# Performance work log

Hardware: AMD Instinct MI355X
Metric: run time of the kernel (lower is better)

## Reference

```python
import jax, jax.numpy as jnp
import numpy as np

E, H = 1024, 16


def setup_inputs() -> dict:
    key = jax.random.key(0)
    k1, k2, k3, k4 = jax.random.split(key, 4)
    B, L = 4, 2048
    embeddings = jax.random.normal(k1, (B, L, E), dtype=jnp.float32)
    mask = jax.random.randint(k2, (B, L, L), 0, 2) == 1  # True = masked out
    # Params (torch Linear y = x @ W.T; we store already-transposed [in, out])
    W_qkv = jax.random.normal(k3, (E, 3 * E), dtype=jnp.float32) * 0.02
    W_out = jax.random.normal(k4, (E, E), dtype=jnp.float32) * 0.02
    return {"embeddings": embeddings, "mask": mask, "W_qkv": W_qkv, "W_out": W_out}


def reference(embeddings, mask, W_qkv, W_out):
    B, L, E_ = embeddings.shape
    A = E_ // H
    scale = A ** (-0.5)
    qkv = embeddings @ W_qkv                       # [B, L, 3E]
    qkv = qkv.reshape(B, L, H, 3 * A).transpose(0, 2, 1, 3)  # [B, H, L, 3A]
    q, k, v = jnp.split(qkv, 3, axis=-1)           # each [B, H, L, A]
    scores = jnp.einsum('bhqa,bhka->bhqk', q, k) * scale  # [B, H, L, L]
    m = mask[:, None, :, :]                        # [B, 1, L, L]
    fully = jnp.all(m, axis=-1, keepdims=True)     # rows with every key masked
    scores = jnp.where(m, -jnp.inf, scores)
    scores = jnp.where(fully, 0.0, scores)         # keep softmax finite
    attn = jax.nn.softmax(scores, axis=-1)
    attn = jnp.where(fully, 0.0, attn)             # == torch nan_to_num(0)
    values = jnp.einsum('bhqk,bhka->bhqa', attn, v)  # [B, H, L, A]
    values = values.transpose(0, 2, 1, 3).reshape(B, L, E_)
    return values @ W_out
```

## Files before the change

### kernel.cpp

```cpp
#include <hip/hip_runtime.h>
#include <hip/hip_bf16.h>

#define B_   4
#define L_   2048
#define E_   1024
#define H_   16
#define T_   8192
#define K_   1024

typedef __attribute__((ext_vector_type(8))) short bf16x8;
typedef __attribute__((ext_vector_type(4))) float f32x4;

#define CSC_ (0.125f * 1.44269504f)

__device__ __forceinline__ ushort f2b(float f) {
    union { float f; unsigned u; } x; x.f = f;
    unsigned r = (x.u + 0x7fffu + ((x.u >> 16) & 1u)) >> 16;
    return (ushort)r;
}

__device__ __forceinline__ float fexp2(float x) {
#if __has_builtin(__builtin_amdgcn_exp2f)
    return __builtin_amdgcn_exp2f(x);
#else
    return __expf(x * 0.69314718056f);
#endif
}

__device__ __forceinline__ unsigned pack2bf(float a, float b) {
#if __has_builtin(__builtin_amdgcn_cvt_pk_bf16_f32)
    auto t = __builtin_amdgcn_cvt_pk_bf16_f32(a, b);
    return __builtin_bit_cast(unsigned, t);
#else
    unsigned ua = __builtin_bit_cast(unsigned, a) + 0x8000u;
    unsigned ub = __builtin_bit_cast(unsigned, b) + 0x8000u;
    return __builtin_amdgcn_perm(ub, ua, 0x07060302);
#endif
}

#define GLD_LDS16(gp, lp) __builtin_amdgcn_global_load_lds( \
    (const __attribute__((address_space(1))) void*)(gp), \
    (__attribute__((address_space(3))) void*)(lp), 16, 0, 0)

__global__ void detect_mask_layout(const unsigned char* __restrict__ m, int* flag) {
    __shared__ int s;
    if (threadIdx.x == 0) s = 0;
    __syncthreads();
    int found = 0;
    for (int i = threadIdx.x; i < 4096; i += 256)
        if ((i & 3) != 0 && m[i] != 0) found = 1;
    if (found) atomicOr(&s, 1);
    __syncthreads();
    if (threadIdx.x == 0) *flag = s;
}

__global__ void pack_mask(const void* __restrict__ mraw, const int* __restrict__ flag,
                          unsigned long long* __restrict__ bits) {
    int row  = blockIdx.x;
    int lane = threadIdx.x & 63;
    int wave = threadIdx.x >> 6;
    int isByte = *flag;
    const unsigned char* mb = (const unsigned char*)mraw;
    const int*           mi = (const int*)mraw;
    long long base = (long long)row * L_;
    for (int w = wave; w < 32; w += 4) {
        int idx = w * 64 + lane;
        int v = isByte ? (int)mb[base + idx] : mi[base + idx];
        unsigned long long word = __ballot(v == 0);
        if (lane == 0) bits[row * 32 + w] = word;
    }
}

__global__ __launch_bounds__(256) void conv_bf16(const float* __restrict__ in,
                                                 ushort* __restrict__ out) {
    int i = blockIdx.x * 256 + threadIdx.x;
    float4 v = ((const float4*)in)[i];
    uint2 o;
    o.x = (unsigned)f2b(v.x) | ((unsigned)f2b(v.y) << 16);
    o.y = (unsigned)f2b(v.z) | ((unsigned)f2b(v.w) << 16);
    ((uint2*)out)[i] = o;
}

__global__ __launch_bounds__(256) void transpose_conv(const float* __restrict__ in,
        ushort* __restrict__ out, int R, int Cn) {
    __shared__ float t[32][33];
    int c0 = blockIdx.x * 32, r0 = blockIdx.y * 32;
    int x = threadIdx.x & 31, y = threadIdx.x >> 5;
#pragma unroll
    for (int k = 0; k < 4; ++k)
        t[y + k * 8][x] = in[(size_t)(r0 + y + k * 8) * Cn + c0 + x];
    __syncthreads();
#pragma unroll
    for (int k = 0; k < 4; ++k)
        out[(size_t)(c0 + y + k * 8) * R + r0 + x] = f2b(t[x][y + k * 8]);
}

template<int NDIM, int MODE>
__global__ __launch_bounds__(256) void gemm_bf16(
        const ushort* __restrict__ Ab, const ushort* __restrict__ Bt,
        float* __restrict__ Cg, ushort* __restrict__ Qb,
        ushort* __restrict__ Kb, ushort* __restrict__ Vt) {
    __shared__ ushort As[128 * 64];
    __shared__ ushort Bs[128 * 64];
    const int tid = threadIdx.x;
    const int wv = tid >> 6, ln = tid & 63;
    const int bn = blockIdx.x * 128, bm = blockIdx.y * 128;
    const int wm = (wv & 1) * 64, wn = (wv >> 1) * 64;
    const int row16 = ln & 15, quad = ln >> 4;
    const int cg8 = (((ln & 7) ^ (ln >> 3)) * 8);

    f32x4 acc[4][4];
#pragma unroll
    for (int i = 0; i < 4; ++i)
#pragma unroll
        for (int j = 0; j < 4; ++j) acc[i][j] = (f32x4){0.f, 0.f, 0.f, 0.f};

    for (int k0 = 0; k0 < K_; k0 += 64) {
        __syncthreads();
#pragma unroll
        for (int it = 0; it < 4; ++it) {
            int rA = wv * 32 + it * 8 + (ln >> 3);
            GLD_LDS16(Ab + (size_t)(bm + rA) * K_ + k0 + cg8, &As[(wv * 32 + it * 8) * 64]);
            GLD_LDS16(Bt + (size_t)(bn + rA) * K_ + k0 + cg8, &Bs[(wv * 32 + it * 8) * 64]);
        }
        __syncthreads();
#pragma unroll
        for (int ks = 0; ks < 2; ++ks) {
            const int ch = (((ks * 4 + quad) ^ (ln & 7)) * 8);
            bf16x8 af[4], bf[4];
#pragma unroll
            for (int i = 0; i < 4; ++i)
                af[i] = *(const bf16x8*)&As[(wm + i * 16 + row16) * 64 + ch];
#pragma unroll
            for (int j = 0; j < 4; ++j)
                bf[j] = *(const bf16x8*)&Bs[(wn + j * 16 + row16) * 64 + ch];
#pragma unroll
            for (int i = 0; i < 4; ++i)
#pragma unroll
                for (int j = 0; j < 4; ++j)
                    acc[i][j] = __builtin_amdgcn_mfma_f32_16x16x32_bf16(
                        af[i], bf[j], acc[i][j], 0, 0, 0);
        }
    }

    if (MODE == 0) {
#pragma unroll
        for (int i = 0; i < 4; ++i)
#pragma unroll
            for (int j = 0; j < 4; ++j) {
                int col = bn + wn + j * 16 + row16;
#pragma unroll
                for (int r = 0; r < 4; ++r) {
                    int row = bm + wm + i * 16 + quad * 4 + r;
                    Cg[(size_t)row * NDIM + col] = acc[i][j][r];
                }
            }
    } else {
#pragma unroll
        for (int j = 0; j < 4; ++j) {
            int col = bn + wn + j * 16 + row16;
            int h = col / 192, w = col - h * 192;
            int sel = w >> 6, a = w & 63;
            float qs = (sel == 0) ? CSC_ : 1.0f;
#pragma unroll
            for (int i = 0; i < 4; ++i)
#pragma unroll
                for (int r = 0; r < 4; ++r) {
                    int rowg = bm + wm + i * 16 + quad * 4 + r;
                    int b = rowg >> 11, l = rowg & 2047;
                    ushort v = f2b(acc[i][j][r] * qs);
                    size_t bh = (size_t)(b * H_ + h);
                    if (sel == 0)      Qb[(bh * L_ + l) * 64 + a] = v;
                    else if (sel == 1) Kb[(bh * L_ + l) * 64 + a] = v;
                    else {
                        int k5 = l & 31;
                        int lp = (l & ~31) | (2 * (k5 & 15) + (k5 >> 4));
                        Vt[(bh * 64 + a) * L_ + lp] = v;
                    }
                }
        }
    }
}

__global__ __launch_bounds__(256) void attn_mfma(
        const ushort* __restrict__ Qb, const ushort* __restrict__ Kb,
        const ushort* __restrict__ Vt, const unsigned* __restrict__ bits32,
        ushort* __restrict__ vals) {
    __shared__ ushort KV[4][2048];
    __shared__ ushort Ps[4][1280];

    const int tid = threadIdx.x, wv = tid >> 6, ln = tid & 63;
    const int bh = blockIdx.y, b = bh >> 4, h = bh & 15;
    const int q0 = blockIdx.x * 128;
    const int row16 = ln & 15, quad = ln >> 4;
    const int lh = ln >> 3, ll = ln & 7;
    const int cg8 = ((ll ^ lh) * 8);

    const ushort* Kg = Kb + (size_t)bh * L_ * 64;
    const ushort* Vg = Vt + (size_t)bh * 64 * L_;

    const int vc = ll ^ lh;
    const ushort* vsrc = Vg + (size_t)(wv * 8 + lh + 32 * (vc >> 2)) * L_ + (vc & 3) * 8;
    const ushort* ksrc = Kg + (size_t)(wv * 8 + lh) * 64 + cg8;

    {
        const ushort* Qgw = Qb + ((size_t)bh * L_ + q0 + wv * 32) * 64;
#pragma unroll
        for (int it = 0; it < 4; ++it)
            GLD_LDS16(Qgw + (size_t)(it * 8 + lh) * 64 + cg8, &KV[wv][it * 8 * 64]);
    }
    __syncthreads();
    bf16x8 aq[2][2];
#pragma unroll
    for (int rg = 0; rg < 2; ++rg)
#pragma unroll
        for (int ks = 0; ks < 2; ++ks)
            aq[rg][ks] = *(const bf16x8*)&KV[wv][(rg * 16 + row16) * 64 +
                                                 (((ks * 4 + quad) ^ (row16 & 7)) * 8)];
    __syncthreads();

    GLD_LDS16(ksrc, &KV[0][(wv * 8) * 64]);
    GLD_LDS16(vsrc, &KV[2][(wv * 8) * 64]);

    ushort* Pw = Ps[wv];
    bf16x8 vone;
#pragma unroll
    for (int i = 0; i < 8; ++i) vone[i] = (short)0x3F80;

    f32x4 oacc[2][4], lacc[2];
#pragma unroll
    for (int rg = 0; rg < 2; ++rg) {
        lacc[rg] = (f32x4){0.f, 0.f, 0.f, 0.f};
#pragma unroll
        for (int t = 0; t < 4; ++t) oacc[rg][t] = (f32x4){0.f, 0.f, 0.f, 0.f};
    }

    const unsigned* mp0 = bits32 + ((size_t)b * L_ + q0 + wv * 32 + quad * 4) * 64;
    const unsigned* mp1 = mp0 + 16 * 64;

    for (int kt = 0; kt < 64; ++kt) {
        const int cur = kt & 1;
        __syncthreads();
        if (kt + 1 < 64) {
            GLD_LDS16(ksrc + (size_t)(kt + 1) * 2048, &KV[cur ^ 1][(wv * 8) * 64]);
            GLD_LDS16(vsrc + (size_t)(kt + 1) * 32,   &KV[2 + (cur ^ 1)][(wv * 8) * 64]);
        }
        unsigned w0[4], w1[4];
#pragma unroll
        for (int r = 0; r < 4; ++r) { w0[r] = mp0[r * 64 + kt]; w1[r] = mp1[r * 64 + kt]; }

        f32x4 sa[2][2];
#pragma unroll
        for (int rg = 0; rg < 2; ++rg)
#pragma unroll
            for (int t = 0; t < 2; ++t) sa[rg][t] = (f32x4){0.f, 0.f, 0.f, 0.f};
#pragma unroll
        for (int ks = 0; ks < 2; ++ks) {
            bf16x8 bk[2];
#pragma unroll
            for (int t = 0; t < 2; ++t)
                bk[t] = *(const bf16x8*)&KV[cur][(t * 16 + row16) * 64 +
                                                 (((ks * 4 + quad) ^ (row16 & 7)) * 8)];
#pragma unroll
            for (int rg = 0; rg < 2; ++rg)
#pragma unroll
                for (int t = 0; t < 2; ++t)
                    sa[rg][t] = __builtin_amdgcn_mfma_f32_16x16x32_bf16(
                        aq[rg][ks], bk[t], sa[rg][t], 0, 0, 0);
        }

#pragma unroll
        for (int rg = 0; rg < 2; ++rg) {
            const unsigned* wr = rg ? w1 : w0;
#pragma unroll
            for (int r = 0; r < 4; ++r) {
                unsigned sh = wr[r] >> row16;
                unsigned pk = pack2bf(fexp2(sa[rg][0][r]), fexp2(sa[rg][1][r]));
                pk &= (sh & 0x00010001u) * 0xFFFFu;
                *(unsigned*)&Pw[(rg * 16 + quad * 4 + r) * 40 + 2 * row16] = pk;
            }
        }

        {
            bf16x8 bv[4];
#pragma unroll
            for (int t = 0; t < 4; ++t)
                bv[t] = *(const bf16x8*)&KV[2 + cur][((t & 1) * 16 + row16) * 64 +
                                                    ((((t >> 1) * 4 + quad) ^ (row16 & 7)) * 8)];
#pragma unroll
            for (int rg = 0; rg < 2; ++rg) {
                bf16x8 ap = *(const bf16x8*)&Pw[(rg * 16 + row16) * 40 + quad * 8];
                lacc[rg] = __builtin_amdgcn_mfma_f32_16x16x32_bf16(ap, vone, lacc[rg], 0, 0, 0);
#pragma unroll
                for (int t = 0; t < 4; ++t)
                    oacc[rg][t] = __builtin_amdgcn_mfma_f32_16x16x32_bf16(
                        ap, bv[t], oacc[rg][t], 0, 0, 0);
            }
        }
    }

#pragma unroll
    for (int rg = 0; rg < 2; ++rg)
#pragma unroll
        for (int r = 0; r < 4; ++r) {
            float l = lacc[rg][r];
            float inv = (l > 0.f) ? 1.0f / l : 0.f;
            int qrow = q0 + wv * 32 + rg * 16 + quad * 4 + r;
            size_t base = ((size_t)b * L_ + qrow) * E_ + h * 64;
#pragma unroll
            for (int t = 0; t < 4; ++t)
                vals[base + t * 16 + row16] = f2b(oacc[rg][t][r] * inv);
        }
}

extern "C" void kernel_launch(void* const* d_in, const int* in_sizes, int n_in,
                              void* d_out, int out_size, void* d_ws, size_t ws_size,
                              hipStream_t stream) {
    const float* emb  = (const float*)d_in[0];
    const void*  mask = d_in[1];
    const float* wqkv = (const float*)d_in[2];
    const float* wout = (const float*)d_in[3];
    float* out = (float*)d_out;

    char* ws = (char*)d_ws;
    const size_t NEED = 4096ull + 2097152ull + 2ull * 46137344ull;
    if (ws_size < NEED) return;

    int* flag = (int*)ws;
    unsigned long long* bits = (unsigned long long*)(ws + 4096);
    ushort* embb  = (ushort*)(ws + 4096 + 2097152);
    ushort* Wqkvt = embb  + 8388608;
    ushort* Wott  = Wqkvt + 3145728;
    ushort* Qb    = Wott  + 1048576;
    ushort* Kb    = Qb    + 8388608;
    ushort* Vt    = Kb    + 8388608;
    ushort* vals  = Vt    + 8388608;

    detect_mask_layout<<<1, 256, 0, stream>>>((const unsigned char*)mask, flag);
    pack_mask<<<T_, 256, 0, stream>>>(mask, flag, bits);
    conv_bf16<<<8192, 256, 0, stream>>>(emb, embb);
    transpose_conv<<<dim3(96, 32), 256, 0, stream>>>(wqkv, Wqkvt, 1024, 3072);
    transpose_conv<<<dim3(32, 32), 256, 0, stream>>>(wout, Wott, 1024, 1024);
    gemm_bf16<3072, 1><<<dim3(24, 64), 256, 0, stream>>>(
        embb, Wqkvt, nullptr, Qb, Kb, Vt);
    attn_mfma<<<dim3(16, 64), 256, 0, stream>>>(
        Qb, Kb, Vt, (const unsigned*)bits, vals);
    gemm_bf16<1024, 0><<<dim3(8, 64), 256, 0, stream>>>(
        vals, Wott, out, nullptr, nullptr, nullptr);
}
```

Baseline: 412.1 us.

## Triple-buffer K/V tiles, software-pipeline QK ahead of softmax-PV, transpose mask bits

The attention loop now keeps three LDS buffers for K and V and prefetches two tiles ahead. It also computes QK scores for the next tile before doing softmax and PV on the current one, so MFMA work from adjacent iterations can interleave. The packed mask is stored transposed (key-word major, query contiguous), which lets each wave load its mask words with vector uint4 loads, prefetched one tile ahead. The cost is more LDS per block, which may reduce occupancy, and higher register pressure from holding two score sets at once.

```diff
diff --git a/kernel.cpp b/kernel.cpp
--- a/kernel.cpp
+++ b/kernel.cpp
@@ -55,11 +55,12 @@
 }
 
 __global__ void pack_mask(const void* __restrict__ mraw, const int* __restrict__ flag,
-                          unsigned long long* __restrict__ bits) {
+                          unsigned* __restrict__ tbits) {
     int row  = blockIdx.x;
     int lane = threadIdx.x & 63;
     int wave = threadIdx.x >> 6;
     int isByte = *flag;
+    int b = row >> 11, q = row & 2047;
     const unsigned char* mb = (const unsigned char*)mraw;
     const int*           mi = (const int*)mraw;
     long long base = (long long)row * L_;
@@ -67,7 +68,10 @@
         int idx = w * 64 + lane;
         int v = isByte ? (int)mb[base + idx] : mi[base + idx];
         unsigned long long word = __ballot(v == 0);
-        if (lane == 0) bits[row * 32 + w] = word;
+        if (lane == 0) {
+            tbits[((size_t)b * 64 + 2 * w)     * 2048 + q] = (unsigned)word;
+            tbits[((size_t)b * 64 + 2 * w + 1) * 2048 + q] = (unsigned)(word >> 32);
+        }
     }
 }
 
@@ -184,9 +188,9 @@
 
 __global__ __launch_bounds__(256) void attn_mfma(
         const ushort* __restrict__ Qb, const ushort* __restrict__ Kb,
-        const ushort* __restrict__ Vt, const unsigned* __restrict__ bits32,
+        const ushort* __restrict__ Vt, const unsigned* __restrict__ tbits,
         ushort* __restrict__ vals) {
-    __shared__ ushort KV[4][2048];
+    __shared__ ushort KV[6][2048];
     __shared__ ushort Ps[4][1280];
 
     const int tid = threadIdx.x, wv = tid >> 6, ln = tid & 63;
@@ -199,8 +203,8 @@
     const ushort* Kg = Kb + (size_t)bh * L_ * 64;
     const ushort* Vg = Vt + (size_t)bh * 64 * L_;
 
-    const int vc = ll ^ lh;
-    const ushort* vsrc = Vg + (size_t)(wv * 8 + lh + 32 * (vc >> 2)) * L_ + (vc & 3) * 8;
+    const int vc4 = ll ^ lh;
+    const ushort* vsrc = Vg + (size_t)(wv * 8 + lh + 32 * (vc4 >> 2)) * L_ + (vc4 & 3) * 8;
     const ushort* ksrc = Kg + (size_t)(wv * 8 + lh) * 64 + cg8;
 
     {
@@ -219,8 +223,15 @@
                                                  (((ks * 4 + quad) ^ (row16 & 7)) * 8)];
     __syncthreads();
 
-    GLD_LDS16(ksrc, &KV[0][(wv * 8) * 64]);
-    GLD_LDS16(vsrc, &KV[2][(wv * 8) * 64]);
+    GLD_LDS16(ksrc,        &KV[0][(wv * 8) * 64]);
+    GLD_LDS16(ksrc + 2048, &KV[1][(wv * 8) * 64]);
+    GLD_LDS16(vsrc,        &KV[3][(wv * 8) * 64]);
+    GLD_LDS16(vsrc + 32,   &KV[4][(wv * 8) * 64]);
+
+    ushort *kc = KV[0], *kn = KV[1], *kf = KV[2];
+    ushort *vcb = KV[3], *vnb = KV[4], *vfb = KV[5];
+    const ushort* kstage = ksrc + 2 * 2048;
+    const ushort* vstage = vsrc + 2 * 32;
 
     ushort* Pw = Ps[wv];
     bf16x8 vone;
@@ -235,43 +246,33 @@
         for (int t = 0; t < 4; ++t) oacc[rg][t] = (f32x4){0.f, 0.f, 0.f, 0.f};
     }
 
-    const unsigned* mp0 = bits32 + ((size_t)b * L_ + q0 + wv * 32 + quad * 4) * 64;
-    const unsigned* mp1 = mp0 + 16 * 64;
-
-    for (int kt = 0; kt < 64; ++kt) {
-        const int cur = kt & 1;
-        __syncthreads();
-        if (kt + 1 < 64) {
-            GLD_LDS16(ksrc + (size_t)(kt + 1) * 2048, &KV[cur ^ 1][(wv * 8) * 64]);
-            GLD_LDS16(vsrc + (size_t)(kt + 1) * 32,   &KV[2 + (cur ^ 1)][(wv * 8) * 64]);
-        }
-        unsigned w0[4], w1[4];
-#pragma unroll
-        for (int r = 0; r < 4; ++r) { w0[r] = mp0[r * 64 + kt]; w1[r] = mp1[r * 64 + kt]; }
-
-        f32x4 sa[2][2];
+    const unsigned* mptr = tbits + (size_t)b * 64 * 2048 + (q0 + wv * 32 + quad * 4);
+
+    auto qk = [&](const ushort* kbuf, f32x4 (&s)[2][2]) {
 #pragma unroll
         for (int rg = 0; rg < 2; ++rg)
 #pragma unroll
-            for (int t = 0; t < 2; ++t) sa[rg][t] = (f32x4){0.f, 0.f, 0.f, 0.f};
+            for (int t = 0; t < 2; ++t) s[rg][t] = (f32x4){0.f, 0.f, 0.f, 0.f};
 #pragma unroll
         for (int ks = 0; ks < 2; ++ks) {
             bf16x8 bk[2];
 #pragma unroll
             for (int t = 0; t < 2; ++t)
-                bk[t] = *(const bf16x8*)&KV[cur][(t * 16 + row16) * 64 +
-                                                 (((ks * 4 + quad) ^ (row16 & 7)) * 8)];
+                bk[t] = *(const bf16x8*)&kbuf[(t * 16 + row16) * 64 +
+                                              (((ks * 4 + quad) ^ (row16 & 7)) * 8)];
 #pragma unroll
             for (int rg = 0; rg < 2; ++rg)
 #pragma unroll
                 for (int t = 0; t < 2; ++t)
-                    sa[rg][t] = __builtin_amdgcn_mfma_f32_16x16x32_bf16(
-                        aq[rg][ks], bk[t], sa[rg][t], 0, 0, 0);
-        }
-
+                    s[rg][t] = __builtin_amdgcn_mfma_f32_16x16x32_bf16(
+                        aq[rg][ks], bk[t], s[rg][t], 0, 0, 0);
+        }
+    };
+
+    auto softmax_pv = [&](f32x4 (&sa)[2][2], uint4 m0, uint4 m1) {
 #pragma unroll
         for (int rg = 0; rg < 2; ++rg) {
-            const unsigned* wr = rg ? w1 : w0;
+            const unsigned* wr = rg ? (const unsigned*)&m1 : (const unsigned*)&m0;
 #pragma unroll
             for (int r = 0; r < 4; ++r) {
                 unsigned sh = wr[r] >> row16;
@@ -280,24 +281,54 @@
                 *(unsigned*)&Pw[(rg * 16 + quad * 4 + r) * 40 + 2 * row16] = pk;
             }
         }
-
-        {
-            bf16x8 bv[4];
+        bf16x8 bv[4];
+#pragma unroll
+        for (int t = 0; t < 4; ++t)
+            bv[t] = *(const bf16x8*)&vcb[((t & 1) * 16 + row16) * 64 +
+                                         ((((t >> 1) * 4 + quad) ^ (row16 & 7)) * 8)];
+#pragma unroll
+        for (int rg = 0; rg < 2; ++rg) {
+            bf16x8 ap = *(const bf16x8*)&Pw[(rg * 16 + row16) * 40 + quad * 8];
+            lacc[rg] = __builtin_amdgcn_mfma_f32_16x16x32_bf16(ap, vone, lacc[rg], 0, 0, 0);
 #pragma unroll
             for (int t = 0; t < 4; ++t)
-                bv[t] = *(const bf16x8*)&KV[2 + cur][((t & 1) * 16 + row16) * 64 +
-                                                    ((((t >> 1) * 4 + quad) ^ (row16 & 7)) * 8)];
-#pragma unroll
-            for (int rg = 0; rg < 2; ++rg) {
-                bf16x8 ap = *(const bf16x8*)&Pw[(rg * 16 + row16) * 40 + quad * 8];
-                lacc[rg] = __builtin_amdgcn_mfma_f32_16x16x32_bf16(ap, vone, lacc[rg], 0, 0, 0);
-#pragma unroll
-                for (int t = 0; t < 4; ++t)
-                    oacc[rg][t] = __builtin_amdgcn_mfma_f32_16x16x32_bf16(
-                        ap, bv[t], oacc[rg][t], 0, 0, 0);
-            }
-        }
-    }
+                oacc[rg][t] = __builtin_amdgcn_mfma_f32_16x16x32_bf16(
+                    ap, bv[t], oacc[rg][t], 0, 0, 0);
+        }
+    };
+
+    auto body = [&](bool do_stage, f32x4 (&sa)[2][2], f32x4 (&sn)[2][2],
+                    uint4 (&mc)[2], uint4 (&mn)[2]) {
+        mn[0] = *(const uint4*)(mptr);
+        mn[1] = *(const uint4*)(mptr + 16);
+        mptr += 2048;
+        if (do_stage) {
+            GLD_LDS16(kstage, &kf[(wv * 8) * 64]);
+            GLD_LDS16(vstage, &vfb[(wv * 8) * 64]);
+            kstage += 2048; vstage += 32;
+        }
+        qk(kn, sn);
+        softmax_pv(sa, mc[0], mc[1]);
+        __syncthreads();
+        ushort* t;
+        t = kc;  kc  = kn;  kn  = kf;  kf  = t;
+        t = vcb; vcb = vnb; vnb = vfb; vfb = t;
+    };
+
+    uint4 mA[2], mB[2];
+    mA[0] = *(const uint4*)(mptr);
+    mA[1] = *(const uint4*)(mptr + 16);
+    mptr += 2048;
+    f32x4 sA[2][2], sB[2][2];
+    __syncthreads();
+    qk(kc, sA);
+
+    for (int i = 0; i < 31; ++i) {
+        body(true, sA, sB, mA, mB);
+        body(2 * i + 1 < 62, sB, sA, mB, mA);
+    }
+    body(false, sA, sB, mA, mB);
+    softmax_pv(sB, mB[0], mB[1]);
 
 #pragma unroll
     for (int rg = 0; rg < 2; ++rg)
@@ -327,7 +358,7 @@
     if (ws_size < NEED) return;
 
     int* flag = (int*)ws;
-    unsigned long long* bits = (unsigned long long*)(ws + 4096);
+    unsigned* tbits = (unsigned*)(ws + 4096);
     ushort* embb  = (ushort*)(ws + 4096 + 2097152);
     ushort* Wqkvt = embb  + 8388608;
     ushort* Wott  = Wqkvt + 3145728;
@@ -337,14 +368,13 @@
     ushort* vals  = Vt    + 8388608;
 
     detect_mask_layout<<<1, 256, 0, stream>>>((const unsigned char*)mask, flag);
-    pack_mask<<<T_, 256, 0, stream>>>(mask, flag, bits);
+    pack_mask<<<T_, 256, 0, stream>>>(mask, flag, tbits);
     conv_bf16<<<8192, 256, 0, stream>>>(emb, embb);
     transpose_conv<<<dim3(96, 32), 256, 0, stream>>>(wqkv, Wqkvt, 1024, 3072);
     transpose_conv<<<dim3(32, 32), 256, 0, stream>>>(wout, Wott, 1024, 1024);
     gemm_bf16<3072, 1><<<dim3(24, 64), 256, 0, stream>>>(
         embb, Wqkvt, nullptr, Qb, Kb, Vt);
-    attn_mfma<<<dim3(16, 64), 256, 0, stream>>>(
-        Qb, Kb, Vt, (const unsigned*)bits, vals);
+    attn_mfma<<<dim3(16, 64), 256, 0, stream>>>(Qb, Kb, Vt, tbits, vals);
     gemm_bf16<1024, 0><<<dim3(8, 64), 256, 0, stream>>>(
         vals, Wott, out, nullptr, nullptr, nullptr);
 }
```

Result: faster. 390.9 us (-5.1%).
